# Optimization experiments

Measured on AMD Instinct MI355X. Metric: run time of the kernel, lower is better.

## Reference

```python
import jax, jax.numpy as jnp
import numpy as np
from jax import lax

EPS = 1e-5
GROUPS = 16


def group_norm(x, gamma, beta, g=GROUPS, eps=EPS):
    B, C, H, W = x.shape
    xr = x.reshape(B, g, C // g, H, W)
    mu = xr.mean(axis=(2, 3, 4), keepdims=True)
    var = xr.var(axis=(2, 3, 4), keepdims=True)
    xn = ((xr - mu) / jnp.sqrt(var + eps)).reshape(B, C, H, W)
    return xn * gamma[None, :, None, None] + beta[None, :, None, None]


def silu(x):
    return x * jax.nn.sigmoid(x)


def recurrence(a, b, c, d, x, axis):
    # h_t = a_t*h_{t-1} + b_t*x_t ; y_t = c_t*h_t + d_t*x_t, scanned along `axis`.
    mv = lambda t: jnp.moveaxis(t, axis, 0)
    def step(h, inp):
        at, bt, ct, dt, xt = inp
        h = at * h + bt * xt
        return h, ct * h + dt * xt
    xs = tuple(map(mv, (a, b, c, d, x)))
    h0 = jnp.zeros_like(xs[4][0])
    _, ys = lax.scan(step, h0, xs)
    return jnp.moveaxis(ys, 0, axis)


def dir_scan(x, wd, bd, axis, flip):
    # Conv1d(c,4c,1) over the scan sequence == pointwise channel linear on NCHW.
    xin = jnp.flip(x, axis) if flip else x
    coeff = jnp.einsum('oc,bchw->bohw', wd, xin) + bd[None, :, None, None]
    C = x.shape[1]
    a, b, c, d = (coeff[:, i * C:(i + 1) * C] for i in range(4))
    a = jax.nn.sigmoid(a)
    y = recurrence(a, b, c, d, xin, axis)
    return jnp.flip(y, axis) if flip else y


def setup_inputs() -> dict:
    key = jax.random.key(0)
    ks = jax.random.split(key, 10)
    B, C, H, W = 4, 128, 128, 128
    s = 1.0 / np.sqrt(C)
    inp = {
        'x': jax.random.normal(ks[0], (B, C, H, W), jnp.float32),
        'w_in': jax.random.normal(ks[1], (C, C), jnp.float32) * s,
        'gn1_gamma': jnp.ones((C,), jnp.float32),
        'gn1_beta': jnp.zeros((C,), jnp.float32),
        'w_gate': jax.random.normal(ks[2], (C, C), jnp.float32) * s,
        'b_gate': jax.random.normal(ks[3], (C,), jnp.float32) * 0.1,
        'dyn_w': jax.random.normal(ks[4], (4, 4 * C, C), jnp.float32) * s,
        'dyn_b': jax.random.normal(ks[5], (4, 4 * C), jnp.float32) * 0.1,
        'dw_kernel': jax.random.normal(ks[6], (C, 1, 3, 3), jnp.float32) * (1.0 / 3.0),
        'w_out': jax.random.normal(ks[7], (C, C), jnp.float32) * s,
        'gn2_gamma': jnp.ones((C,), jnp.float32),
        'gn2_beta': jnp.zeros((C,), jnp.float32),
    }
    return inp


def reference(x, w_in, gn1_gamma, gn1_beta, w_gate, b_gate, dyn_w, dyn_b,
              dw_kernel, w_out, gn2_gamma, gn2_beta):
    C = x.shape[1]
    # in_proj: 1x1 conv (no bias) -> GroupNorm -> SiLU
    xp = jnp.einsum('oc,bchw->bohw', w_in, x)
    xp = silu(group_norm(xp, gn1_gamma, gn1_beta))
    # 4-directional dynamic selective scans
    y_lr = dir_scan(xp, dyn_w[0], dyn_b[0], axis=3, flip=False)
    y_rl = dir_scan(xp, dyn_w[1], dyn_b[1], axis=3, flip=True)
    y_tb = dir_scan(xp, dyn_w[2], dyn_b[2], axis=2, flip=False)
    y_bt = dir_scan(xp, dyn_w[3], dyn_b[3], axis=2, flip=True)
    fused = 0.25 * (y_lr + y_rl + y_tb + y_bt)
    # gate: 1x1 conv + bias -> sigmoid, applied to projected x
    gate = jax.nn.sigmoid(jnp.einsum('oc,bchw->bohw', w_gate, xp)
                          + b_gate[None, :, None, None])
    z = fused * gate
    # out_proj: depthwise 3x3 -> 1x1 conv -> GroupNorm -> SiLU
    z = lax.conv_general_dilated(z, dw_kernel, (1, 1), ((1, 1), (1, 1)),
                                 feature_group_count=C,
                                 dimension_numbers=('NCHW', 'OIHW', 'NCHW'))
    z = jnp.einsum('oc,bchw->bohw', w_out, z)
    return silu(group_norm(z, gn2_gamma, gn2_beta))
```

## Files before the change

kernel.cpp:

```cpp
#include <hip/hip_runtime.h>
#include <math.h>

#define B_ 4
#define C_ 128
#define HW_ 16384
#define P_ 65536
#define S_ 8388608
#define CPG 8

typedef unsigned short u16;
typedef __attribute__((ext_vector_type(8))) short short8;
typedef __attribute__((ext_vector_type(4))) float f32x4;

__device__ __forceinline__ float sigmoidf_(float x){ return 1.f/(1.f+__expf(-x)); }
__device__ __forceinline__ float siluf_(float x){ return x*sigmoidf_(x); }
__device__ __forceinline__ u16 f2bf(float f){
  unsigned x = __float_as_uint(f);
  return (u16)((x + 0x7fffu + ((x >> 16) & 1u)) >> 16);
}
__device__ __forceinline__ float b2f(u16 u){ return __uint_as_float(((unsigned)u) << 16); }

__global__ __launch_bounds__(256) void prep_kernel(const float* __restrict__ dyn_w,
    const float* __restrict__ dyn_b, const float* __restrict__ w_gate,
    const float* __restrict__ w_out, const float* __restrict__ w_in,
    u16* __restrict__ wfrag, float* __restrict__ bperm, u16* __restrict__ wgbf,
    u16* __restrict__ wobf, u16* __restrict__ wibf, float* __restrict__ stats)
{
  int idx = blockIdx.x*256 + threadIdx.x;
  if (idx < 262144) {
    int e = idx & 7, lane = (idx >> 3) & 63, kk = (idx >> 9) & 3;
    int ct = (idx >> 11) & 31, d = idx >> 16;
    int m = lane & 15, kg = lane >> 4;
    int col = ct*16 + m;
    int c = col >> 2, f = col & 3;
    int k = kk*32 + kg*8 + e;
    wfrag[idx] = f2bf(dyn_w[(size_t)((d*512) + f*128 + c)*128 + k]);
  } else if (idx < 264192) {
    int i2 = idx - 262144;
    int op = i2 & 511, d = i2 >> 9;
    bperm[i2] = dyn_b[d*512 + (op & 3)*128 + (op >> 2)];
  } else if (idx < 280576) {
    wgbf[idx - 264192] = f2bf(w_gate[idx - 264192]);
  } else if (idx < 296960) {
    wobf[idx - 280576] = f2bf(w_out[idx - 280576]);
  } else if (idx < 313344) {
    wibf[idx - 296960] = f2bf(w_in[idx - 296960]);
  } else if (idx < 313600) {
    stats[idx - 313344] = 0.f;
  }
}

__global__ __launch_bounds__(256) void mfma_inproj(const float* __restrict__ x,
    const u16* __restrict__ Wm, u16* __restrict__ Out)
{
  __shared__ __align__(16) u16 st[64*136];
  int t = threadIdx.x;
  int wv = t >> 6, lane = t & 63;
  int m = lane & 15, kg = lane >> 4;
  int pt = blockIdx.x << 6;
  int b = blockIdx.x >> 8;
  int hw0 = (blockIdx.x & 255) << 6;
  const float* xb = x + ((size_t)b << 21);

  short8 Af[4][4];
  #pragma unroll
  for (int rt = 0; rt < 4; ++rt) {
    int pos = hw0 + rt*16 + m;
    #pragma unroll
    for (int kk = 0; kk < 4; ++kk) {
      short8 f;
      #pragma unroll
      for (int e = 0; e < 8; ++e)
        f[e] = (short)f2bf(xb[(size_t)(kk*32 + kg*8 + e)*HW_ + pos]);
      Af[rt][kk] = f;
    }
  }
  #pragma unroll
  for (int ct2 = 0; ct2 < 2; ++ct2) {
    int ot = wv*32 + ct2*16;
    const u16* wr = Wm + ((size_t)(ot + m) << 7) + kg*8;
    short8 Bf[4];
    #pragma unroll
    for (int kk = 0; kk < 4; ++kk)
      Bf[kk] = *(const short8*)(wr + kk*32);
    f32x4 acc[4];
    #pragma unroll
    for (int rt = 0; rt < 4; ++rt) acc[rt] = (f32x4){0.f,0.f,0.f,0.f};
    #pragma unroll
    for (int rt = 0; rt < 4; ++rt)
      #pragma unroll
      for (int kk = 0; kk < 4; ++kk)
        acc[rt] = __builtin_amdgcn_mfma_f32_16x16x32_bf16(Af[rt][kk], Bf[kk], acc[rt], 0, 0, 0);
    #pragma unroll
    for (int rt = 0; rt < 4; ++rt) {
      #pragma unroll
      for (int r = 0; r < 4; ++r)
        st[(rt*16 + kg*4 + r)*136 + ot + m] = f2bf(acc[rt][r]);
    }
  }
  __syncthreads();
  #pragma unroll
  for (int i = 0; i < 4; ++i) {
    int slot = i*256 + t;
    int row = slot >> 4, j = slot & 15;
    short8 v = *(const short8*)(st + row*136 + (j << 3));
    *(short8*)(Out + ((size_t)(pt + row) << 7) + (j << 3)) = v;
  }
}

template<int BIAS, int SIG>
__global__ __launch_bounds__(256) void mfma_nt128(const u16* __restrict__ X,
    const u16* __restrict__ Wm, const float* __restrict__ bias, u16* __restrict__ Out)
{
  __shared__ __align__(16) u16 st[64*136];
  int t = threadIdx.x;
  int wv = t >> 6, lane = t & 63;
  int m = lane & 15, kg = lane >> 4;
  int pt = blockIdx.x << 6;

  short8 Af[4][4];
  #pragma unroll
  for (int rt = 0; rt < 4; ++rt) {
    const u16* ar = X + ((size_t)(pt + rt*16 + m) << 7) + kg*8;
    #pragma unroll
    for (int kk = 0; kk < 4; ++kk)
      Af[rt][kk] = *(const short8*)(ar + kk*32);
  }
  #pragma unroll
  for (int ct2 = 0; ct2 < 2; ++ct2) {
    int ot = wv*32 + ct2*16;
    const u16* wr = Wm + ((size_t)(ot + m) << 7) + kg*8;
    short8 Bf[4];
    #pragma unroll
    for (int kk = 0; kk < 4; ++kk)
      Bf[kk] = *(const short8*)(wr + kk*32);
    f32x4 acc[4];
    #pragma unroll
    for (int rt = 0; rt < 4; ++rt) acc[rt] = (f32x4){0.f,0.f,0.f,0.f};
    #pragma unroll
    for (int rt = 0; rt < 4; ++rt)
      #pragma unroll
      for (int kk = 0; kk < 4; ++kk)
        acc[rt] = __builtin_amdgcn_mfma_f32_16x16x32_bf16(Af[rt][kk], Bf[kk], acc[rt], 0, 0, 0);
    float bv = BIAS ? bias[ot + m] : 0.f;
    #pragma unroll
    for (int rt = 0; rt < 4; ++rt) {
      #pragma unroll
      for (int r = 0; r < 4; ++r) {
        float v = acc[rt][r] + bv;
        if (SIG) v = sigmoidf_(v);
        st[(rt*16 + kg*4 + r)*136 + ot + m] = f2bf(v);
      }
    }
  }
  __syncthreads();
  #pragma unroll
  for (int i = 0; i < 4; ++i) {
    int slot = i*256 + t;
    int row = slot >> 4, j = slot & 15;
    short8 v = *(const short8*)(st + row*136 + (j << 3));
    *(short8*)(Out + ((size_t)(pt + row) << 7) + (j << 3)) = v;
  }
}

#define PRODUCE(NT, bufv, chunkv)  do { \
  int posg_ = (chunkv)*16 + m; int swp_ = (posg_ & 7) << 4; \
  short8 Bfr[4]; \
  _Pragma("unroll") for (int kk = 0; kk < 4; ++kk) \
    Bfr[kk] = *(const short8*)((char*)xs + posg_*256 + (((kk<<6)+(kg<<4)) ^ swp_)); \
  _Pragma("unroll") for (int ti = 0; ti < NT; ++ti) { \
    f32x4 acc = (f32x4){0.f,0.f,0.f,0.f}; \
    _Pragma("unroll") for (int kk = 0; kk < 4; ++kk) \
      acc = __builtin_amdgcn_mfma_f32_16x16x32_bf16(Af[ti][kk], Bfr[kk], acc, 0, 0, 0); \
    int colL_ = (tbase + ti)*16 + (kg<<2); \
    unsigned lo_ = (unsigned)f2bf(acc[0]) | ((unsigned)f2bf(acc[1])<<16); \
    unsigned hi_ = (unsigned)f2bf(acc[2]) | ((unsigned)f2bf(acc[3])<<16); \
    int byte_ = (((bufv)*2 + dw)<<14) + (m<<10) + ((colL_<<1) ^ ((m&7)<<4)); \
    *(uint2*)((char*)cs + byte_) = make_uint2(lo_, hi_); \
  } } while(0)

#define SCAN_STEP(s) { \
  float ar = b2f((u16)(cw[s].x & 0xffffu)) + bv.x; \
  float br = b2f((u16)(cw[s].x >> 16)) + bv.y; \
  float cr = b2f((u16)(cw[s].y & 0xffffu)) + bv.z; \
  float dr = b2f((u16)(cw[s].y >> 16)) + bv.w; \
  float aa = sigmoidf_(ar); \
  h = aa*h + br*xf[s]; \
  yv[s] = cr*h + dr*xf[s]; }

template<int AXISW, int PART>
__global__ __launch_bounds__(512, 2) void scan_fused(const u16* __restrict__ Abf,
    const u16* __restrict__ Wf, const float* __restrict__ bias,
    u16* __restrict__ fusedP)
{
  __shared__ __align__(16) u16 xs[128*128];
  __shared__ __align__(16) u16 cs[2][2][16*512];
  __shared__ __align__(16) u16 ysL[128*128];
  int line = blockIdx.x;
  int b = line >> 7, l = line & 127;
  int t = threadIdx.x;
  int wv = t >> 6, lane = t & 63;
  int m = lane & 15, kg = lane >> 4;
  int dw = (wv >> 1) & 1;

  #pragma unroll
  for (int i = 0; i < 4; ++i) {
    int idx = i*512 + t;
    int pos = idx >> 4, j = idx & 15;
    size_t row = AXISW ? ((size_t)(b<<14) + (l<<7) + pos)
                       : ((size_t)(b<<14) + (pos<<7) + l);
    short8 v = *(const short8*)(Abf + (row<<7) + (j<<3));
    int byte = pos*256 + ((j*16) ^ ((pos&7)<<4));
    *(short8*)((char*)xs + byte) = v;
  }

  if (wv < 4) {
    int tbase = (wv & 1) * 4;
    short8 Af[4][4];
    #pragma unroll
    for (int ti = 0; ti < 4; ++ti)
      #pragma unroll
      for (int kk = 0; kk < 4; ++kk)
        Af[ti][kk] = *(const short8*)(Wf + (size_t)(((dw*32 + tbase + ti)*4 + kk)*64 + lane)*8);
    __syncthreads();
    PRODUCE(4, 0, dw ? 7 : 0);
    __syncthreads();

    int sd = dw;
    int sc = ((wv & 1) << 6) + lane;
    float4 bv = *(const float4*)(bias + (sd << 9) + (sc << 2));
    float h = 0.f;

    #pragma unroll 1
    for (int k = 0; k < 8; ++k) {
      if (k < 7) PRODUCE(4, (k+1)&1, dw ? (6-k) : (k+1));
      int chunk = sd ? (7-k) : k;
      int csb = (((k&1)*2 + sd) << 14);
      uint2 cw[16];
      #pragma unroll
      for (int s = 0; s < 16; ++s)
        cw[s] = *(const uint2*)((char*)cs + csb + (s<<10) + ((sc<<3) ^ ((s&7)<<4)));
      float xf[16];
      #pragma unroll
      for (int s = 0; s < 16; ++s) {
        int pos = (chunk<<4) + s;
        xf[s] = b2f(*(const u16*)((char*)xs + pos*256 + ((sc<<1) ^ ((s&7)<<4))));
      }
      float yv[16];
      __builtin_amdgcn_s_setprio(1);
      if (sd == 0) {
        #pragma unroll
        for (int s = 0; s < 16; ++s) SCAN_STEP(s)
      } else {
        #pragma unroll
        for (int s = 15; s >= 0; --s) SCAN_STEP(s)
      }
      __builtin_amdgcn_s_setprio(0);
      u16* yrow = ysL + (chunk << 11) + sc;
      if (k <= 3) {
        #pragma unroll
        for (int s = 0; s < 16; ++s) yrow[s << 7] = f2bf(0.25f*yv[s]);
      } else {
        #pragma unroll
        for (int s = 0; s < 16; ++s) {
          float o = b2f(yrow[s << 7]);
          yrow[s << 7] = f2bf(o + 0.25f*yv[s]);
        }
      }
      __syncthreads();
    }
  } else {
    int tbase = 8 + (wv & 1) * 12;
    short8 Af[12][4];
    #pragma unroll
    for (int ti = 0; ti < 12; ++ti)
      #pragma unroll
      for (int kk = 0; kk < 4; ++kk)
        Af[ti][kk] = *(const short8*)(Wf + (size_t)(((dw*32 + tbase + ti)*4 + kk)*64 + lane)*8);
    __syncthreads();
    PRODUCE(12, 0, dw ? 7 : 0);
    __syncthreads();
    #pragma unroll 1
    for (int k = 0; k < 8; ++k) {
      if (k < 7) PRODUCE(12, (k+1)&1, dw ? (6-k) : (k+1));
      __syncthreads();
    }
  }

  #pragma unroll
  for (int r = 0; r < 4; ++r) {
    int slot = r*512 + t;
    int pos = slot >> 4, j = slot & 15;
    short8 v = *(const short8*)(ysL + (pos << 7) + (j << 3));
    size_t rowg = AXISW ? ((size_t)(b<<14) + (l<<7) + pos)
                        : ((size_t)(b<<14) + (pos<<7) + l);
    u16* op = fusedP + (rowg << 7) + (j << 3);
    if (PART) {
      short8 o = *(const short8*)op;
      short8 rr;
      #pragma unroll
      for (int i = 0; i < 8; ++i) rr[i] = (short)f2bf(b2f((u16)v[i]) + b2f((u16)o[i]));
      *(short8*)op = rr;
    } else {
      *(short8*)op = v;
    }
  }
}

__global__ __launch_bounds__(256) void gn_stats_bf(const u16* __restrict__ X,
    float* __restrict__ stats)
{
  int b = blockIdx.x, chunk = blockIdx.y;
  const u16* base = X + ((size_t)b << 21) + ((size_t)chunk << 15);
  int t = threadIdx.x;
  float s = 0.f, q = 0.f;
  #pragma unroll 4
  for (int it = 0; it < 16; ++it) {
    short8 v = *(const short8*)(base + it*2048 + t*8);
    #pragma unroll
    for (int e = 0; e < 8; ++e) { float f = b2f((u16)v[e]); s += f; q += f*f; }
  }
  s += __shfl_xor(s, 16); q += __shfl_xor(q, 16);
  s += __shfl_xor(s, 32); q += __shfl_xor(q, 32);
  __shared__ float sg[32];
  if (t < 32) sg[t] = 0.f;
  __syncthreads();
  int lane = t & 63;
  if (lane < 16) { atomicAdd(&sg[lane], s); atomicAdd(&sg[16 + lane], q); }
  __syncthreads();
  if (t < 16) atomicAdd(&stats[b*16 + t], sg[t]);
  else if (t < 32) atomicAdd(&stats[64 + b*16 + (t - 16)], sg[t]);
}

__global__ __launch_bounds__(256) void gn_apply(const u16* __restrict__ X,
    const float* __restrict__ stats, const float* __restrict__ gamma,
    const float* __restrict__ beta, u16* __restrict__ Xb)
{
  int i4 = blockIdx.x*256 + threadIdx.x;
  size_t base = (size_t)i4 << 2;
  int c4 = (int)(base & 127);
  size_t p = base >> 7;
  int b = (int)(p >> 14);
  int g = c4 >> 3;
  const float cnt = (float)(CPG*HW_);
  float mu = stats[b*16+g]/cnt;
  float var = stats[64+b*16+g]/cnt - mu*mu;
  float rs = rsqrtf(var + 1e-5f);
  ushort4 v = *(const ushort4*)(X + base);
  ushort4 o;
  o.x = f2bf(siluf_((b2f(v.x)-mu)*rs*gamma[c4+0]+beta[c4+0]));
  o.y = f2bf(siluf_((b2f(v.y)-mu)*rs*gamma[c4+1]+beta[c4+1]));
  o.z = f2bf(siluf_((b2f(v.z)-mu)*rs*gamma[c4+2]+beta[c4+2]));
  o.w = f2bf(siluf_((b2f(v.w)-mu)*rs*gamma[c4+3]+beta[c4+3]));
  *(ushort4*)(Xb + base) = o;
}

__global__ __launch_bounds__(256) void dwconv(const u16* __restrict__ Z,
    const u16* __restrict__ G, const float* __restrict__ K9, u16* __restrict__ Outp)
{
  __shared__ float kk[1152];
  int t = threadIdx.x;
  for (int i = t; i < 1152; i += 256) kk[i] = K9[i];
  __syncthreads();
  int i4 = blockIdx.x*256 + t;
  size_t base = (size_t)i4 << 2;
  int c0 = (int)(base & 127);
  size_t p = base >> 7;
  int w = (int)(p & 127), h = (int)((p >> 7) & 127), b = (int)(p >> 14);
  float4 acc = make_float4(0.f,0.f,0.f,0.f);
  #pragma unroll
  for (int di = 0; di < 3; ++di) {
    int hy = h + di - 1;
    if ((unsigned)hy > 127u) continue;
    #pragma unroll
    for (int dj = 0; dj < 3; ++dj) {
      int wx = w + dj - 1;
      if ((unsigned)wx > 127u) continue;
      size_t p2 = ((size_t)b << 14) + (hy << 7) + wx;
      ushort4 zv = *(const ushort4*)(Z + (p2 << 7) + c0);
      ushort4 gv = *(const ushort4*)(G + (p2 << 7) + c0);
      int o = di*3 + dj;
      acc.x += b2f(zv.x) * b2f(gv.x) * kk[c0*9 + o];
      acc.y += b2f(zv.y) * b2f(gv.y) * kk[(c0+1)*9 + o];
      acc.z += b2f(zv.z) * b2f(gv.z) * kk[(c0+2)*9 + o];
      acc.w += b2f(zv.w) * b2f(gv.w) * kk[(c0+3)*9 + o];
    }
  }
  ushort4 ov;
  ov.x = f2bf(acc.x); ov.y = f2bf(acc.y); ov.z = f2bf(acc.z); ov.w = f2bf(acc.w);
  *(ushort4*)(Outp + base) = ov;
}

__global__ __launch_bounds__(256) void gn_final(const u16* __restrict__ Z,
    const float* __restrict__ stats, const float* __restrict__ gamma,
    const float* __restrict__ beta, float* __restrict__ out)
{
  __shared__ float ls[32][129];
  int w0 = blockIdx.x << 5, hh = blockIdx.y, b = blockIdx.z;
  size_t p0 = ((size_t)b << 14) + (hh << 7) + w0;
  int t = threadIdx.x;
  const float cnt = (float)(CPG*HW_);
  #pragma unroll
  for (int i = 0; i < 4; ++i) {
    int l = t + i*256;
    int row = l >> 5, c4 = (l & 31) << 2;
    ushort4 v = *(const ushort4*)(Z + ((p0 + row) << 7) + c4);
    int g = c4 >> 3;
    float mu = stats[b*16+g]/cnt;
    float var = stats[64+b*16+g]/cnt - mu*mu;
    float rs = rsqrtf(var + 1e-5f);
    float vals[4] = {b2f(v.x), b2f(v.y), b2f(v.z), b2f(v.w)};
    #pragma unroll
    for (int j = 0; j < 4; ++j) {
      float nv = (vals[j]-mu)*rs*gamma[c4+j] + beta[c4+j];
      ls[row][c4+j] = siluf_(nv);
    }
  }
  __syncthreads();
  int ww = t & 31, c0 = t >> 5;
  #pragma unroll
  for (int cc = c0; cc < 128; cc += 8) {
    out[(((size_t)(b*128 + cc)) << 14) + (hh << 7) + (w0 + ww)] = ls[ww][cc];
  }
}

extern "C" void kernel_launch(void* const* d_in, const int* in_sizes, int n_in,
                              void* d_out, int out_size, void* d_ws, size_t ws_size,
                              hipStream_t stream)
{
  (void)in_sizes; (void)n_in; (void)out_size; (void)ws_size;
  const float* x      = (const float*)d_in[0];
  const float* w_in   = (const float*)d_in[1];
  const float* g1g    = (const float*)d_in[2];
  const float* g1b    = (const float*)d_in[3];
  const float* w_gate = (const float*)d_in[4];
  const float* b_gate = (const float*)d_in[5];
  const float* dyn_w  = (const float*)d_in[6];
  const float* dyn_b  = (const float*)d_in[7];
  const float* dwk    = (const float*)d_in[8];
  const float* w_out  = (const float*)d_in[9];
  const float* g2g    = (const float*)d_in[10];
  const float* g2b    = (const float*)d_in[11];
  float* out = (float*)d_out;

  char* p = (char*)d_ws;
  u16*   Zbuf   = (u16*)p;              p += (size_t)S_*2;
  u16*   xpr    = (u16*)p;              p += (size_t)S_*2;
  u16*   Abf    = (u16*)p;              p += (size_t)S_*2;
  u16*   fusedP = (u16*)p;              p += (size_t)S_*2;
  u16*   Gbf    = (u16*)p;              p += (size_t)S_*2;
  u16*   wfrag  = (u16*)p;              p += (size_t)262144*2;
  u16*   wgbf   = (u16*)p;              p += (size_t)16384*2;
  u16*   wobf   = (u16*)p;              p += (size_t)16384*2;
  u16*   wibf   = (u16*)p;              p += (size_t)16384*2;
  float* bperm  = (float*)p;            p += (size_t)2048*4;
  float* stats  = (float*)p;            p += (size_t)256*4;
  u16*   Zdw    = Zbuf;
  u16*   Zout   = xpr;

  prep_kernel<<<1225, 256, 0, stream>>>(dyn_w, dyn_b, w_gate, w_out, w_in,
                                        wfrag, bperm, wgbf, wobf, wibf, stats);
  mfma_inproj<<<1024, 256, 0, stream>>>(x, wibf, xpr);
  gn_stats_bf<<<dim3(4, 64), 256, 0, stream>>>(xpr, stats);
  gn_apply<<<8192, 256, 0, stream>>>(xpr, stats, g1g, g1b, Abf);

  scan_fused<1,0><<<512, 512, 0, stream>>>(Abf, wfrag, bperm, fusedP);
  scan_fused<0,1><<<512, 512, 0, stream>>>(Abf, wfrag + 131072, bperm + 1024, fusedP);

  mfma_nt128<1,1><<<1024, 256, 0, stream>>>(Abf, wgbf, b_gate, Gbf);
  dwconv<<<8192, 256, 0, stream>>>(fusedP, Gbf, dwk, Zdw);
  mfma_nt128<0,0><<<1024, 256, 0, stream>>>(Zdw, wobf, nullptr, Zout);
  gn_stats_bf<<<dim3(4, 64), 256, 0, stream>>>(Zout, stats + 128);
  gn_final<<<dim3(4, 128, 4), 256, 0, stream>>>(Zout, stats + 128, g2g, g2b, out);
}
```

Measured before the change: 199.1 us.

## Split bidirectional scan blocks into one direction per block with separate outputs

Each scan block used to handle both directions of a line, with 4 scanner waves and 4 producer waves computing coefficients for both. Now each block handles one direction, so the grid doubles to 1024 blocks. All 8 waves compute coefficients and only 2 waves run the sequential scan. The forward and reverse results go to separate buffers, and the depthwise-conv kernel reads both and sums them. This trades more total blocks and extra memory traffic (a second intermediate buffer read in dwconv) for more parallelism and a shorter critical path per block.

```diff
diff --git a/kernel.cpp b/kernel.cpp
--- a/kernel.cpp
+++ b/kernel.cpp
@@ -163,19 +163,19 @@
   }
 }
 
-#define PRODUCE(NT, bufv, chunkv)  do { \
+#define PRODUCE2(chunkv, bufv)  do { \
   int posg_ = (chunkv)*16 + m; int swp_ = (posg_ & 7) << 4; \
   short8 Bfr[4]; \
   _Pragma("unroll") for (int kk = 0; kk < 4; ++kk) \
     Bfr[kk] = *(const short8*)((char*)xs + posg_*256 + (((kk<<6)+(kg<<4)) ^ swp_)); \
-  _Pragma("unroll") for (int ti = 0; ti < NT; ++ti) { \
+  _Pragma("unroll") for (int ti = 0; ti < 4; ++ti) { \
     f32x4 acc = (f32x4){0.f,0.f,0.f,0.f}; \
     _Pragma("unroll") for (int kk = 0; kk < 4; ++kk) \
       acc = __builtin_amdgcn_mfma_f32_16x16x32_bf16(Af[ti][kk], Bfr[kk], acc, 0, 0, 0); \
     int colL_ = (tbase + ti)*16 + (kg<<2); \
     unsigned lo_ = (unsigned)f2bf(acc[0]) | ((unsigned)f2bf(acc[1])<<16); \
     unsigned hi_ = (unsigned)f2bf(acc[2]) | ((unsigned)f2bf(acc[3])<<16); \
-    int byte_ = (((bufv)*2 + dw)<<14) + (m<<10) + ((colL_<<1) ^ ((m&7)<<4)); \
+    int byte_ = ((bufv)<<14) + (m<<10) + ((colL_<<1) ^ ((m&7)<<4)); \
     *(uint2*)((char*)cs + byte_) = make_uint2(lo_, hi_); \
   } } while(0)
 
@@ -189,19 +189,22 @@
   yv[s] = cr*h + dr*xf[s]; }
 
 template<int AXISW, int PART>
-__global__ __launch_bounds__(512, 2) void scan_fused(const u16* __restrict__ Abf,
-    const u16* __restrict__ Wf, const float* __restrict__ bias,
-    u16* __restrict__ fusedP)
+__global__ __launch_bounds__(512, 2) void scan_dir(const u16* __restrict__ Abf,
+    const u16* __restrict__ Wfbase, const float* __restrict__ biasbase,
+    u16* __restrict__ fusedA, u16* __restrict__ fusedB)
 {
   __shared__ __align__(16) u16 xs[128*128];
-  __shared__ __align__(16) u16 cs[2][2][16*512];
+  __shared__ __align__(16) u16 cs[2][16*512];
   __shared__ __align__(16) u16 ysL[128*128];
-  int line = blockIdx.x;
+  int dir = blockIdx.x >> 9;
+  int line = blockIdx.x & 511;
   int b = line >> 7, l = line & 127;
   int t = threadIdx.x;
   int wv = t >> 6, lane = t & 63;
   int m = lane & 15, kg = lane >> 4;
-  int dw = (wv >> 1) & 1;
+  const u16* Wf = Wfbase + dir*65536;
+  const float* bias = biasbase + dir*512;
+  u16* dst = dir ? fusedB : fusedA;
 
   #pragma unroll
   for (int i = 0; i < 4; ++i) {
@@ -214,28 +217,29 @@
     *(short8*)((char*)xs + byte) = v;
   }
 
-  if (wv < 4) {
-    int tbase = (wv & 1) * 4;
-    short8 Af[4][4];
-    #pragma unroll
-    for (int ti = 0; ti < 4; ++ti)
-      #pragma unroll
-      for (int kk = 0; kk < 4; ++kk)
-        Af[ti][kk] = *(const short8*)(Wf + (size_t)(((dw*32 + tbase + ti)*4 + kk)*64 + lane)*8);
-    __syncthreads();
-    PRODUCE(4, 0, dw ? 7 : 0);
-    __syncthreads();
-
-    int sd = dw;
-    int sc = ((wv & 1) << 6) + lane;
-    float4 bv = *(const float4*)(bias + (sd << 9) + (sc << 2));
-    float h = 0.f;
-
-    #pragma unroll 1
-    for (int k = 0; k < 8; ++k) {
-      if (k < 7) PRODUCE(4, (k+1)&1, dw ? (6-k) : (k+1));
-      int chunk = sd ? (7-k) : k;
-      int csb = (((k&1)*2 + sd) << 14);
+  int tbase = wv << 2;
+  short8 Af[4][4];
+  #pragma unroll
+  for (int ti = 0; ti < 4; ++ti)
+    #pragma unroll
+    for (int kk = 0; kk < 4; ++kk)
+      Af[ti][kk] = *(const short8*)(Wf + (size_t)(((tbase + ti)*4 + kk)*64 + lane)*8);
+
+  __syncthreads();
+  PRODUCE2(dir ? 7 : 0, 0);
+  __syncthreads();
+
+  int sc = (wv << 6) + lane;
+  float4 bv = make_float4(0.f,0.f,0.f,0.f);
+  if (wv < 2) bv = *(const float4*)(bias + (sc << 2));
+  float h = 0.f;
+
+  #pragma unroll 1
+  for (int k = 0; k < 8; ++k) {
+    if (k < 7) PRODUCE2(dir ? (6-k) : (k+1), (k+1)&1);
+    if (wv < 2) {
+      int chunk = dir ? (7-k) : k;
+      int csb = (k & 1) << 14;
       uint2 cw[16];
       #pragma unroll
       for (int s = 0; s < 16; ++s)
@@ -248,7 +252,7 @@
       }
       float yv[16];
       __builtin_amdgcn_s_setprio(1);
-      if (sd == 0) {
+      if (dir == 0) {
         #pragma unroll
         for (int s = 0; s < 16; ++s) SCAN_STEP(s)
       } else {
@@ -257,34 +261,10 @@
       }
       __builtin_amdgcn_s_setprio(0);
       u16* yrow = ysL + (chunk << 11) + sc;
-      if (k <= 3) {
-        #pragma unroll
-        for (int s = 0; s < 16; ++s) yrow[s << 7] = f2bf(0.25f*yv[s]);
-      } else {
-        #pragma unroll
-        for (int s = 0; s < 16; ++s) {
-          float o = b2f(yrow[s << 7]);
-          yrow[s << 7] = f2bf(o + 0.25f*yv[s]);
-        }
-      }
-      __syncthreads();
-    }
-  } else {
-    int tbase = 8 + (wv & 1) * 12;
-    short8 Af[12][4];
-    #pragma unroll
-    for (int ti = 0; ti < 12; ++ti)
-      #pragma unroll
-      for (int kk = 0; kk < 4; ++kk)
-        Af[ti][kk] = *(const short8*)(Wf + (size_t)(((dw*32 + tbase + ti)*4 + kk)*64 + lane)*8);
+      #pragma unroll
+      for (int s = 0; s < 16; ++s) yrow[s << 7] = f2bf(0.25f*yv[s]);
+    }
     __syncthreads();
-    PRODUCE(12, 0, dw ? 7 : 0);
-    __syncthreads();
-    #pragma unroll 1
-    for (int k = 0; k < 8; ++k) {
-      if (k < 7) PRODUCE(12, (k+1)&1, dw ? (6-k) : (k+1));
-      __syncthreads();
-    }
   }
 
   #pragma unroll
@@ -294,7 +274,7 @@
     short8 v = *(const short8*)(ysL + (pos << 7) + (j << 3));
     size_t rowg = AXISW ? ((size_t)(b<<14) + (l<<7) + pos)
                         : ((size_t)(b<<14) + (pos<<7) + l);
-    u16* op = fusedP + (rowg << 7) + (j << 3);
+    u16* op = dst + (rowg << 7) + (j << 3);
     if (PART) {
       short8 o = *(const short8*)op;
       short8 rr;
@@ -355,8 +335,9 @@
   *(ushort4*)(Xb + base) = o;
 }
 
-__global__ __launch_bounds__(256) void dwconv(const u16* __restrict__ Z,
-    const u16* __restrict__ G, const float* __restrict__ K9, u16* __restrict__ Outp)
+__global__ __launch_bounds__(256) void dwconv(const u16* __restrict__ ZA,
+    const u16* __restrict__ ZB, const u16* __restrict__ G,
+    const float* __restrict__ K9, u16* __restrict__ Outp)
 {
   __shared__ float kk[1152];
   int t = threadIdx.x;
@@ -377,13 +358,14 @@
       int wx = w + dj - 1;
       if ((unsigned)wx > 127u) continue;
       size_t p2 = ((size_t)b << 14) + (hy << 7) + wx;
-      ushort4 zv = *(const ushort4*)(Z + (p2 << 7) + c0);
+      ushort4 za = *(const ushort4*)(ZA + (p2 << 7) + c0);
+      ushort4 zb = *(const ushort4*)(ZB + (p2 << 7) + c0);
       ushort4 gv = *(const ushort4*)(G + (p2 << 7) + c0);
       int o = di*3 + dj;
-      acc.x += b2f(zv.x) * b2f(gv.x) * kk[c0*9 + o];
-      acc.y += b2f(zv.y) * b2f(gv.y) * kk[(c0+1)*9 + o];
-      acc.z += b2f(zv.z) * b2f(gv.z) * kk[(c0+2)*9 + o];
-      acc.w += b2f(zv.w) * b2f(gv.w) * kk[(c0+3)*9 + o];
+      acc.x += (b2f(za.x)+b2f(zb.x)) * b2f(gv.x) * kk[c0*9 + o];
+      acc.y += (b2f(za.y)+b2f(zb.y)) * b2f(gv.y) * kk[(c0+1)*9 + o];
+      acc.z += (b2f(za.z)+b2f(zb.z)) * b2f(gv.z) * kk[(c0+2)*9 + o];
+      acc.w += (b2f(za.w)+b2f(zb.w)) * b2f(gv.w) * kk[(c0+3)*9 + o];
     }
   }
   ushort4 ov;
@@ -447,7 +429,8 @@
   u16*   Zbuf   = (u16*)p;              p += (size_t)S_*2;
   u16*   xpr    = (u16*)p;              p += (size_t)S_*2;
   u16*   Abf    = (u16*)p;              p += (size_t)S_*2;
-  u16*   fusedP = (u16*)p;              p += (size_t)S_*2;
+  u16*   fusedA = (u16*)p;              p += (size_t)S_*2;
+  u16*   fusedB = (u16*)p;              p += (size_t)S_*2;
   u16*   Gbf    = (u16*)p;              p += (size_t)S_*2;
   u16*   wfrag  = (u16*)p;              p += (size_t)262144*2;
   u16*   wgbf   = (u16*)p;              p += (size_t)16384*2;
@@ -464,11 +447,11 @@
   gn_stats_bf<<<dim3(4, 64), 256, 0, stream>>>(xpr, stats);
   gn_apply<<<8192, 256, 0, stream>>>(xpr, stats, g1g, g1b, Abf);
 
-  scan_fused<1,0><<<512, 512, 0, stream>>>(Abf, wfrag, bperm, fusedP);
-  scan_fused<0,1><<<512, 512, 0, stream>>>(Abf, wfrag + 131072, bperm + 1024, fusedP);
+  scan_dir<1,0><<<1024, 512, 0, stream>>>(Abf, wfrag,            bperm,        fusedA, fusedB);
+  scan_dir<0,1><<<1024, 512, 0, stream>>>(Abf, wfrag + 2*65536,  bperm + 1024, fusedA, fusedB);
 
   mfma_nt128<1,1><<<1024, 256, 0, stream>>>(Abf, wgbf, b_gate, Gbf);
-  dwconv<<<8192, 256, 0, stream>>>(fusedP, Gbf, dwk, Zdw);
+  dwconv<<<8192, 256, 0, stream>>>(fusedA, fusedB, Gbf, dwk, Zdw);
   mfma_nt128<0,0><<<1024, 256, 0, stream>>>(Zdw, wobf, nullptr, Zout);
   gn_stats_bf<<<dim3(4, 64), 256, 0, stream>>>(Zout, stats + 128);
   gn_final<<<dim3(4, 128, 4), 256, 0, stream>>>(Zout, stats + 128, g2g, g2b, out);
```

Result: slower. 251.2 us (+26.2%).

## Widen scan_fused blocks to 1024 threads and rebalance MFMA production across waves

Applied to the files above, without the earlier changes.

The fused scan kernel now launches 1024-thread blocks in place of 512. All 16 waves produce 4 MFMA tiles each, where before four scan waves did 4 tiles and four producer waves did 12. The four scan waves also process each 16-step chunk in two halves of 8 to reduce register pressure. The aim is to balance the coefficient-projection work and cut the register footprint per wave. In exchange, only one block fits per CU given the large LDS allocation, and every wave pays extra barrier cost.

```diff
diff --git a/kernel.cpp b/kernel.cpp
--- a/kernel.cpp
+++ b/kernel.cpp
@@ -163,12 +163,12 @@
   }
 }
 
-#define PRODUCE(NT, bufv, chunkv)  do { \
+#define PRODUCE2(chunkv, bufv)  do { \
   int posg_ = (chunkv)*16 + m; int swp_ = (posg_ & 7) << 4; \
   short8 Bfr[4]; \
   _Pragma("unroll") for (int kk = 0; kk < 4; ++kk) \
     Bfr[kk] = *(const short8*)((char*)xs + posg_*256 + (((kk<<6)+(kg<<4)) ^ swp_)); \
-  _Pragma("unroll") for (int ti = 0; ti < NT; ++ti) { \
+  _Pragma("unroll") for (int ti = 0; ti < 4; ++ti) { \
     f32x4 acc = (f32x4){0.f,0.f,0.f,0.f}; \
     _Pragma("unroll") for (int kk = 0; kk < 4; ++kk) \
       acc = __builtin_amdgcn_mfma_f32_16x16x32_bf16(Af[ti][kk], Bfr[kk], acc, 0, 0, 0); \
@@ -189,7 +189,7 @@
   yv[s] = cr*h + dr*xf[s]; }
 
 template<int AXISW, int PART>
-__global__ __launch_bounds__(512, 2) void scan_fused(const u16* __restrict__ Abf,
+__global__ __launch_bounds__(1024) void scan_fused(const u16* __restrict__ Abf,
     const u16* __restrict__ Wf, const float* __restrict__ bias,
     u16* __restrict__ fusedP)
 {
@@ -201,11 +201,13 @@
   int t = threadIdx.x;
   int wv = t >> 6, lane = t & 63;
   int m = lane & 15, kg = lane >> 4;
-  int dw = (wv >> 1) & 1;
-
-  #pragma unroll
-  for (int i = 0; i < 4; ++i) {
-    int idx = i*512 + t;
+  int dw, tbase;
+  if (wv < 4) { dw = (wv >> 1) & 1; tbase = (wv & 1) * 4; }
+  else        { int pw = wv - 4; dw = pw & 1; tbase = 8 + (pw >> 1) * 4; }
+
+  #pragma unroll
+  for (int i = 0; i < 2; ++i) {
+    int idx = i*1024 + t;
     int pos = idx >> 4, j = idx & 15;
     size_t row = AXISW ? ((size_t)(b<<14) + (l<<7) + pos)
                        : ((size_t)(b<<14) + (pos<<7) + l);
@@ -214,82 +216,59 @@
     *(short8*)((char*)xs + byte) = v;
   }
 
-  if (wv < 4) {
-    int tbase = (wv & 1) * 4;
-    short8 Af[4][4];
-    #pragma unroll
-    for (int ti = 0; ti < 4; ++ti)
-      #pragma unroll
-      for (int kk = 0; kk < 4; ++kk)
-        Af[ti][kk] = *(const short8*)(Wf + (size_t)(((dw*32 + tbase + ti)*4 + kk)*64 + lane)*8);
-    __syncthreads();
-    PRODUCE(4, 0, dw ? 7 : 0);
-    __syncthreads();
-
-    int sd = dw;
-    int sc = ((wv & 1) << 6) + lane;
-    float4 bv = *(const float4*)(bias + (sd << 9) + (sc << 2));
-    float h = 0.f;
-
-    #pragma unroll 1
-    for (int k = 0; k < 8; ++k) {
-      if (k < 7) PRODUCE(4, (k+1)&1, dw ? (6-k) : (k+1));
+  short8 Af[4][4];
+  #pragma unroll
+  for (int ti = 0; ti < 4; ++ti)
+    #pragma unroll
+    for (int kk = 0; kk < 4; ++kk)
+      Af[ti][kk] = *(const short8*)(Wf + (size_t)(((dw*32 + tbase + ti)*4 + kk)*64 + lane)*8);
+
+  __syncthreads();
+  PRODUCE2(dw ? 7 : 0, 0);
+  __syncthreads();
+
+  int sd = dw;
+  int sc = ((wv & 1) << 6) + lane;
+  float4 bv = make_float4(0.f, 0.f, 0.f, 0.f);
+  if (wv < 4) bv = *(const float4*)(bias + (sd << 9) + (sc << 2));
+  float h = 0.f;
+
+  #pragma unroll 1
+  for (int k = 0; k < 8; ++k) {
+    if (k < 7) PRODUCE2(dw ? (6-k) : (k+1), (k+1)&1);
+    if (wv < 4) {
       int chunk = sd ? (7-k) : k;
       int csb = (((k&1)*2 + sd) << 14);
-      uint2 cw[16];
-      #pragma unroll
-      for (int s = 0; s < 16; ++s)
-        cw[s] = *(const uint2*)((char*)cs + csb + (s<<10) + ((sc<<3) ^ ((s&7)<<4)));
-      float xf[16];
-      #pragma unroll
-      for (int s = 0; s < 16; ++s) {
-        int pos = (chunk<<4) + s;
-        xf[s] = b2f(*(const u16*)((char*)xs + pos*256 + ((sc<<1) ^ ((s&7)<<4))));
-      }
-      float yv[16];
-      __builtin_amdgcn_s_setprio(1);
-      if (sd == 0) {
+      #pragma unroll
+      for (int hh = 0; hh < 2; ++hh) {
+        uint2 cw[8]; float xf[8];
         #pragma unroll
-        for (int s = 0; s < 16; ++s) SCAN_STEP(s)
-      } else {
+        for (int s = 0; s < 8; ++s) {
+          int posL = sd ? (15 - (hh*8 + s)) : (hh*8 + s);
+          cw[s] = *(const uint2*)((char*)cs + csb + (posL<<10) + ((sc<<3) ^ ((posL&7)<<4)));
+          int pos = (chunk<<4) + posL;
+          xf[s] = b2f(*(const u16*)((char*)xs + pos*256 + ((sc<<1) ^ ((posL&7)<<4))));
+        }
+        float yv[8];
+        __builtin_amdgcn_s_setprio(1);
         #pragma unroll
-        for (int s = 15; s >= 0; --s) SCAN_STEP(s)
-      }
-      __builtin_amdgcn_s_setprio(0);
-      u16* yrow = ysL + (chunk << 11) + sc;
-      if (k <= 3) {
+        for (int s = 0; s < 8; ++s) SCAN_STEP(s)
+        __builtin_amdgcn_s_setprio(0);
         #pragma unroll
-        for (int s = 0; s < 16; ++s) yrow[s << 7] = f2bf(0.25f*yv[s]);
-      } else {
-        #pragma unroll
-        for (int s = 0; s < 16; ++s) {
-          float o = b2f(yrow[s << 7]);
-          yrow[s << 7] = f2bf(o + 0.25f*yv[s]);
+        for (int s = 0; s < 8; ++s) {
+          int posL = sd ? (15 - (hh*8 + s)) : (hh*8 + s);
+          u16* yp = ysL + (((chunk<<4) + posL) << 7) + sc;
+          if (k <= 3) *yp = f2bf(0.25f*yv[s]);
+          else        *yp = f2bf(b2f(*yp) + 0.25f*yv[s]);
         }
       }
-      __syncthreads();
-    }
-  } else {
-    int tbase = 8 + (wv & 1) * 12;
-    short8 Af[12][4];
-    #pragma unroll
-    for (int ti = 0; ti < 12; ++ti)
-      #pragma unroll
-      for (int kk = 0; kk < 4; ++kk)
-        Af[ti][kk] = *(const short8*)(Wf + (size_t)(((dw*32 + tbase + ti)*4 + kk)*64 + lane)*8);
+    }
     __syncthreads();
-    PRODUCE(12, 0, dw ? 7 : 0);
-    __syncthreads();
-    #pragma unroll 1
-    for (int k = 0; k < 8; ++k) {
-      if (k < 7) PRODUCE(12, (k+1)&1, dw ? (6-k) : (k+1));
-      __syncthreads();
-    }
-  }
-
-  #pragma unroll
-  for (int r = 0; r < 4; ++r) {
-    int slot = r*512 + t;
+  }
+
+  #pragma unroll
+  for (int r = 0; r < 2; ++r) {
+    int slot = r*1024 + t;
     int pos = slot >> 4, j = slot & 15;
     short8 v = *(const short8*)(ysL + (pos << 7) + (j << 3));
     size_t rowg = AXISW ? ((size_t)(b<<14) + (l<<7) + pos)
@@ -464,8 +443,8 @@
   gn_stats_bf<<<dim3(4, 64), 256, 0, stream>>>(xpr, stats);
   gn_apply<<<8192, 256, 0, stream>>>(xpr, stats, g1g, g1b, Abf);
 
-  scan_fused<1,0><<<512, 512, 0, stream>>>(Abf, wfrag, bperm, fusedP);
-  scan_fused<0,1><<<512, 512, 0, stream>>>(Abf, wfrag + 131072, bperm + 1024, fusedP);
+  scan_fused<1,0><<<512, 1024, 0, stream>>>(Abf, wfrag, bperm, fusedP);
+  scan_fused<0,1><<<512, 1024, 0, stream>>>(Abf, wfrag + 2*65536, bperm + 1024, fusedP);
 
   mfma_nt128<1,1><<<1024, 256, 0, stream>>>(Abf, wgbf, b_gate, Gbf);
   dwconv<<<8192, 256, 0, stream>>>(fusedP, Gbf, dwk, Zdw);
```

Measured after the change: 316.6 us. 1.59x slower.
